# Optimization experiments

Measured on AMD Instinct MI355X. Metric: run time of the kernel, lower is better.

The kernel has to match this reference:

```python
import jax, jax.numpy as jnp
import numpy as np

B, N_NODES, VOCAB, H = 128, 1023, 2048, 256  # depth-9 perfect binary trees (heap layout)


def setup_inputs() -> dict:
    key = jax.random.key(0)
    k1, k2, k3, k4, k5 = jax.random.split(key, 5)
    tokens = jax.random.randint(k1, (B, N_NODES), 0, VOCAB)
    emb = jax.random.normal(k2, (VOCAB, H), dtype=jnp.float32) * 0.02
    Wx = jax.random.normal(k3, (H, 5 * H), dtype=jnp.float32) * 0.02
    Ul = jax.random.normal(k4, (H, 5 * H), dtype=jnp.float32) * 0.02
    Ur = jax.random.normal(k5, (H, 5 * H), dtype=jnp.float32) * 0.02
    b = jnp.zeros((5 * H,), dtype=jnp.float32)
    return {"tokens": tokens, "emb": emb, "Wx": Wx, "Ul": Ul, "Ur": Ur, "b": b}


def _tree_lstm(tokens, emb, Wx, Ul, Ur, b):
    # tokens: [B, 2^(D+1)-1] in level-order heap layout; children of heap index i
    # are 2i+1, 2i+2 -> within level d+1 they sit at offsets 2k, 2k+1.
    n_nodes = tokens.shape[1]
    depth = int(np.log2(n_nodes + 1)) - 1
    hdim = emb.shape[1]
    x_all = emb[tokens]  # [B, N, H] embedding lookup (memory-bound gather)
    h = c = None
    for d in range(depth, -1, -1):  # bottom-up over levels (fixed structural loop)
        start, n = 2 ** d - 1, 2 ** d
        x = x_all[:, start:start + n]  # [B, n, H]
        gates = jnp.einsum('bnh,hg->bng', x, Wx) + b
        if h is not None:
            hl, hr = h[:, 0::2], h[:, 1::2]
            cl, cr = c[:, 0::2], c[:, 1::2]
            gates = gates + jnp.einsum('bnh,hg->bng', hl, Ul) + jnp.einsum('bnh,hg->bng', hr, Ur)
        i, fl, fr, o, u = jnp.split(gates, 5, axis=-1)
        i, fl, fr, o = map(jax.nn.sigmoid, (i, fl, fr, o))
        u = jnp.tanh(u)
        c_new = i * u
        if c is not None:
            c_new = c_new + fl * cl + fr * cr
        c = c_new
        h = o * jnp.tanh(c)
    return h[:, 0], c[:, 0]  # root states, each [B, H]


def reference(tokens, emb, Wx, Ul, Ur, b):
    h_root, _ = _tree_lstm(tokens, emb, Wx, Ul, Ur, b)
    return h_root  # [B, H]
```

## Files before the change

### kernel.cpp

```cpp
#include <hip/hip_runtime.h>
#include <hip/hip_bf16.h>
#include <math.h>

#define B_SZ   128
#define HDIM   256
#define NG     1280
#define NNODES 1023
#define VOCAB  2048

typedef unsigned int uint32;
typedef short  short8v  __attribute__((ext_vector_type(8)));
typedef float  float4v  __attribute__((ext_vector_type(4)));

__device__ __forceinline__ float sigm(float x) {
    return 1.0f / (1.0f + __expf(-x));
}
__device__ __forceinline__ float tanh_fast(float x) {
    return 2.0f / (1.0f + __expf(-2.0f * x)) - 1.0f;
}
__device__ __forceinline__ float bf2f(unsigned short u) {
    return __uint_as_float(((uint32)u) << 16);
}
__device__ __forceinline__ unsigned short f2bf(float f) {
    uint32 x = __float_as_uint(f);
    uint32 r = (x + 0x7FFFu + ((x >> 16) & 1u)) >> 16;
    return (unsigned short)r;
}

__device__ __forceinline__ void dma16(const unsigned short* gptr, unsigned short* lptr) {
    __builtin_amdgcn_global_load_lds(
        (const __attribute__((address_space(1))) void*)gptr,
        (__attribute__((address_space(3))) void*)lptr, 16, 0, 0);
}

__global__ __launch_bounds__(256) void embb_kernel(
    const float* __restrict__ emb, unsigned short* __restrict__ embb)
{
    const int t = blockIdx.x * 256 + threadIdx.x;
    const float4 v0 = *(const float4*)(emb + (size_t)t * 8);
    const float4 v1 = *(const float4*)(emb + (size_t)t * 8 + 4);
    short8v o;
    o[0] = (short)f2bf(v0.x); o[1] = (short)f2bf(v0.y);
    o[2] = (short)f2bf(v0.z); o[3] = (short)f2bf(v0.w);
    o[4] = (short)f2bf(v1.x); o[5] = (short)f2bf(v1.y);
    o[6] = (short)f2bf(v1.z); o[7] = (short)f2bf(v1.w);
    *(short8v*)(embb + (size_t)t * 8) = o;
}

__global__ __launch_bounds__(256) void prep_wtf(
    const float* __restrict__ Ul, const float* __restrict__ Ur,
    const float* __restrict__ Wx, unsigned short* __restrict__ WTf)
{
    const int t = blockIdx.x * 256 + threadIdx.x;
    const int l = t & 63;
    const int q = l >> 4, c = l & 15;
    const int ks = (t >> 6) % 24;
    const int ng = t / (24 * 64);
    const int col = ng * 16 + c;
    const int k = ks * 32 + q * 8;
    const float* src = (k < 256) ? (Ul + (size_t)k * NG + col)
                     : (k < 512) ? (Ur + (size_t)(k - 256) * NG + col)
                                 : (Wx + (size_t)(k - 512) * NG + col);
    short8v v;
    #pragma unroll
    for (int j = 0; j < 8; ++j) v[j] = (short)f2bf(src[(size_t)j * NG]);
    *(short8v*)(WTf + (size_t)t * 8) = v;
}

__global__ __launch_bounds__(256, 2) void ewb_mfma(
    const unsigned short* __restrict__ WTf, const unsigned short* __restrict__ embb,
    const float* __restrict__ bias, unsigned short* __restrict__ EWb)
{
    __shared__ __align__(16) unsigned short Ab[2][4096];
    __shared__ __align__(16) unsigned short wbE[20480];

    const int tid  = threadIdx.x;
    const int lane = tid & 63;
    const int w    = tid >> 6;
    const int quad = lane >> 4, col15 = lane & 15;
    const int jt = blockIdx.x;
    const int rowBase = blockIdx.y * 64;
    const int jbase   = jt * 64;

    const unsigned short* agp[2];
    unsigned short* ldst[2];
    #pragma unroll
    for (int t = 0; t < 2; ++t) {
        const int ch = 2 * w + t, sub = ch >> 2, rt = ch & 3;
        const int srow = rowBase + rt * 16 + col15;
        agp[t]  = embb + (size_t)srow * HDIM + sub * 32 + quad * 8;
        ldst[t] = &Ab[0][0] + ch * 512;
    }

    const short8v* WTfv = (const short8v*)WTf;
    uint32 boff[5];
    #pragma unroll
    for (int g = 0; g < 5; ++g)
        boff[g] = ((g * 16 + jt * 4 + w) * 24 + 16) * 64 + lane;

    float4v acc[4][5];
    #pragma unroll
    for (int rt = 0; rt < 4; ++rt)
        #pragma unroll
        for (int g = 0; g < 5; ++g)
            #pragma unroll
            for (int e = 0; e < 4; ++e) acc[rt][g][e] = 0.0f;

    dma16(agp[0], ldst[0]); dma16(agp[1], ldst[1]);
    __syncthreads();

    #pragma unroll
    for (int s = 0; s < 4; ++s) {
        if (s < 3) {
            dma16(agp[0] + (s + 1) * 64, ldst[0] + ((s + 1) & 1) * 4096);
            dma16(agp[1] + (s + 1) * 64, ldst[1] + ((s + 1) & 1) * 4096);
        }
        #pragma unroll
        for (int sub = 0; sub < 2; ++sub) {
            short8v bf[5];
            #pragma unroll
            for (int g = 0; g < 5; ++g) bf[g] = WTfv[boff[g] + (s * 2 + sub) * 64];
            #pragma unroll
            for (int rt = 0; rt < 4; ++rt) {
                const short8v af = *(const short8v*)&Ab[s & 1][(sub * 4 + rt) * 512 + lane * 8];
                #pragma unroll
                for (int g = 0; g < 5; ++g)
                    acc[rt][g] = __builtin_amdgcn_mfma_f32_16x16x32_bf16(
                        af, bf[g], acc[rt][g], 0, 0, 0);
            }
        }
        __syncthreads();
    }

    const int jl = w * 16 + col15;
    const int j  = jbase + jl;
    float bz[5];
    #pragma unroll
    for (int g = 0; g < 5; ++g) bz[g] = bias[g * 256 + j];
    const int jchunk = jl >> 3, jpos = jl & 7;

    #pragma unroll
    for (int rt = 0; rt < 4; ++rt) {
        #pragma unroll
        for (int reg = 0; reg < 4; ++reg) {
            const int rr = rt * 16 + quad * 4 + reg;
            const int roff = ((jchunk + 2 * quad) & 7) * 8 + jpos;
            #pragma unroll
            for (int g = 0; g < 5; ++g)
                wbE[(g * 64 + rr) * 64 + roff] = f2bf(acc[rt][g][reg] + bz[g]);
        }
    }
    __syncthreads();

    #pragma unroll
    for (int k2 = 0; k2 < 10; ++k2) {
        const int c = tid + k2 * 256;
        const int g = c >> 9, rr = (c >> 3) & 63, u = c & 7;
        const int ru = (u + 2 * ((rr >> 2) & 3)) & 7;
        const short8v v = *(const short8v*)&wbE[(g * 64 + rr) * 64 + ru * 8];
        *(short8v*)(EWb + (size_t)(rowBase + rr) * NG + g * 256 + jbase + u * 8) = v;
    }
}

__global__ __launch_bounds__(256) void leaftab_kernel(
    const unsigned short* __restrict__ EWb,
    unsigned short* __restrict__ Hleaf, unsigned short* __restrict__ Cleaf)
{
    const int t = blockIdx.x * 256 + threadIdx.x;
    const int tok = t >> 8, j = t & 255;
    const float gi = bf2f(EWb[(size_t)tok * NG + j]);
    const float go = bf2f(EWb[(size_t)tok * NG + 768 + j]);
    const float gu = bf2f(EWb[(size_t)tok * NG + 1024 + j]);
    const float c = sigm(gi) * tanh_fast(gu);
    const float h = sigm(go) * tanh_fast(c);
    Hleaf[t] = f2bf(h);
    Cleaf[t] = f2bf(c);
}

template <bool LEAF>
__global__ __launch_bounds__(256, 2) void level_kernel(
    const unsigned short* __restrict__ WTf, const int* __restrict__ tokens,
    const unsigned short* __restrict__ embb,
    const unsigned short* __restrict__ Hleaf, const unsigned short* __restrict__ Cleaf,
    const unsigned short* __restrict__ hsrc, const unsigned short* __restrict__ csrc,
    const float* __restrict__ bias,
    unsigned short* __restrict__ hdst, unsigned short* __restrict__ cdst,
    float* __restrict__ out, const int d)
{
    const int n = 1 << d;

    __shared__ __align__(16) unsigned short Ab[2][8192];

    const int tid  = threadIdx.x;
    const int lane = tid & 63;
    const int w    = tid >> 6;
    const int quad = lane >> 4, col15 = lane & 15;
    const int jt = blockIdx.x;
    const int rowBase = blockIdx.y * 64;
    const int jbase   = jt * 64;

    const uint32 inrow = (uint32)(w * 64 + quad * 16);
    uint32 oL[4], oR[4], oN[4];
    #pragma unroll
    for (int t = 0; t < 4; ++t) {
        const int srow = rowBase + t * 16 + col15;
        const int b = srow >> d, i = srow & (n - 1);
        oN[t] = (uint32)tokens[b * NNODES + (n - 1) + i] * 512u + inrow;
        if (LEAF) {
            oL[t] = (uint32)tokens[b * NNODES + 511 + 2 * i] * 512u + inrow;
            oR[t] = (uint32)tokens[b * NNODES + 512 + 2 * i] * 512u + inrow;
        } else {
            oL[t] = (uint32)(2 * srow) * 512u + inrow;
            oR[t] = oL[t] + 512u;
        }
    }
    const char* hb = LEAF ? (const char*)Hleaf : (const char*)hsrc;
    const char* xb = (const char*)embb;

    const short8v* WTfv = (const short8v*)WTf;
    uint32 boff[5];
    #pragma unroll
    for (int g = 0; g < 5; ++g)
        boff[g] = ((g * 16 + jt * 4 + w) * 24) * 64 + lane;

    const int jl = w * 16 + col15;
    const int j  = jbase + jl;
    float bz[5];
    #pragma unroll
    for (int g = 0; g < 5; ++g) bz[g] = bias[g * 256 + j];

    float4v acc[4][5];
    #pragma unroll
    for (int rt = 0; rt < 4; ++rt)
        #pragma unroll
        for (int g = 0; g < 5; ++g)
            #pragma unroll
            for (int e = 0; e < 4; ++e) acc[rt][g][e] = 0.0f;

    {
        unsigned short* dst = &Ab[0][0] + w * 2048;
        #pragma unroll
        for (int t = 0; t < 4; ++t)
            dma16((const unsigned short*)(hb + oL[t]), dst + t * 512);
    }
    __syncthreads();

    #pragma unroll
    for (int s = 0; s < 6; ++s) {
        if (s < 5) {
            const int sn = s + 1;
            unsigned short* dst = &Ab[sn & 1][0] + w * 2048;
            #pragma unroll
            for (int t = 0; t < 4; ++t) {
                const char* p = (sn < 2) ? (hb + oL[t] + sn * 256)
                              : (sn < 4) ? (hb + oR[t] + (sn - 2) * 256)
                                         : (xb + oN[t] + (sn - 4) * 256);
                dma16((const unsigned short*)p, dst + t * 512);
            }
        }

        #pragma unroll
        for (int sub = 0; sub < 4; ++sub) {
            short8v bf[5];
            #pragma unroll
            for (int g = 0; g < 5; ++g) bf[g] = WTfv[boff[g] + (s * 4 + sub) * 64];
            #pragma unroll
            for (int rt = 0; rt < 4; ++rt) {
                const short8v af = *(const short8v*)&Ab[s & 1][(sub * 4 + rt) * 512 + lane * 8];
                #pragma unroll
                for (int g = 0; g < 5; ++g)
                    acc[rt][g] = __builtin_amdgcn_mfma_f32_16x16x32_bf16(
                        af, bf[g], acc[rt][g], 0, 0, 0);
            }
        }
        __syncthreads();
    }

    float hv[4][4], cv[4][4];
    #pragma unroll
    for (int rt = 0; rt < 4; ++rt) {
        #pragma unroll
        for (int reg = 0; reg < 4; ++reg) {
            const int rr = rt * 16 + quad * 4 + reg;
            const int grow = rowBase + rr;
            float cl, cr;
            if (LEAF) {
                const int b = grow >> 8, i = grow & 255;
                const int tokL = tokens[b * NNODES + 511 + 2 * i];
                const int tokR = tokens[b * NNODES + 512 + 2 * i];
                cl = bf2f(Cleaf[(size_t)tokL * HDIM + j]);
                cr = bf2f(Cleaf[(size_t)tokR * HDIM + j]);
            } else {
                cl = bf2f(csrc[(size_t)(2 * grow) * HDIM + j]);
                cr = bf2f(csrc[(size_t)(2 * grow + 1) * HDIM + j]);
            }
            const float gi  = acc[rt][0][reg] + bz[0];
            const float gfl = acc[rt][1][reg] + bz[1];
            const float gfr = acc[rt][2][reg] + bz[2];
            const float go  = acc[rt][3][reg] + bz[3];
            const float gu  = acc[rt][4][reg] + bz[4];
            const float ii = sigm(gi), fl = sigm(gfl), fr = sigm(gfr), oo = sigm(go);
            const float uu = tanh_fast(gu);
            const float c = ii * uu + fl * cl + fr * cr;
            const float h = oo * tanh_fast(c);
            cv[rt][reg] = c; hv[rt][reg] = h;
            if (!LEAF && d == 0) out[(size_t)grow * HDIM + j] = h;
        }
    }
    if (!LEAF && d == 0) return;

    unsigned short* wb = &Ab[0][0];
    const int jchunk = jl >> 3, jpos = jl & 7;
    #pragma unroll
    for (int rt = 0; rt < 4; ++rt) {
        #pragma unroll
        for (int reg = 0; reg < 4; ++reg) {
            const int rr = rt * 16 + quad * 4 + reg;
            const int roff = ((jchunk + 2 * quad) & 7) * 8 + jpos;
            wb[rr * 64 + roff]        = f2bf(hv[rt][reg]);
            wb[4096 + rr * 64 + roff] = f2bf(cv[rt][reg]);
        }
    }
    __syncthreads();
    #pragma unroll
    for (int k2 = 0; k2 < 4; ++k2) {
        const int c = tid + k2 * 256;
        const int arr = c >> 9, rr = (c >> 3) & 63, u = c & 7;
        const int ru = (u + 2 * ((rr >> 2) & 3)) & 7;
        const short8v v = *(const short8v*)(wb + (arr * 4096 + rr * 64 + ru * 8));
        unsigned short* dstp = (arr ? cdst : hdst) +
            (size_t)(rowBase + rr) * HDIM + jbase + u * 8;
        *(short8v*)dstp = v;
    }
}

extern "C" void kernel_launch(void* const* d_in, const int* in_sizes, int n_in,
                              void* d_out, int out_size, void* d_ws, size_t ws_size,
                              hipStream_t stream)
{
    const int*   tokens = (const int*)d_in[0];
    const float* emb    = (const float*)d_in[1];
    const float* Wx     = (const float*)d_in[2];
    const float* Ul     = (const float*)d_in[3];
    const float* Ur     = (const float*)d_in[4];
    const float* bias   = (const float*)d_in[5];
    float* out = (float*)d_out;

    const size_t EW_ELEMS  = (size_t)VOCAB * NG;
    const size_t EMB_ELEMS = (size_t)VOCAB * HDIM;
    const size_t WTF_ELEMS = (size_t)80 * 24 * 64 * 8;
    const size_t LT_ELEMS  = (size_t)VOCAB * HDIM;
    const size_t SLOT_A    = (size_t)16384 * HDIM;
    const size_t SLOT_B    = (size_t)32768 * HDIM;
    const size_t REQUIRED  = (EW_ELEMS + EMB_ELEMS + WTF_ELEMS + 2 * LT_ELEMS
                              + 2 * (SLOT_A + SLOT_B)) * 2;
    if (ws_size < REQUIRED || d_ws == nullptr) return;

    char* ws = (char*)d_ws;
    unsigned short* EWb   = (unsigned short*)ws;
    unsigned short* embb  = EWb + EW_ELEMS;
    unsigned short* WTf   = embb + EMB_ELEMS;
    unsigned short* Hleaf = WTf + WTF_ELEMS;
    unsigned short* Cleaf = Hleaf + LT_ELEMS;
    unsigned short* hA    = Cleaf + LT_ELEMS;
    unsigned short* cA    = hA + SLOT_A;
    unsigned short* hB    = cA + SLOT_A;
    unsigned short* cB    = hB + SLOT_B;

    embb_kernel<<<dim3(256), 256, 0, stream>>>(emb, embb);
    prep_wtf<<<dim3(480), 256, 0, stream>>>(Ul, Ur, Wx, WTf);
    ewb_mfma<<<dim3(4, 32), 256, 0, stream>>>(WTf, embb, bias, EWb);
    leaftab_kernel<<<dim3(2048), 256, 0, stream>>>(EWb, Hleaf, Cleaf);

    for (int d = 8; d >= 0; --d) {
        const int NRB = 2 << d;
        const bool evenD = ((d & 1) == 0);
        const unsigned short* hs = evenD ? hA : hB;
        const unsigned short* cs = evenD ? cA : cB;
        unsigned short* hd = evenD ? hB : hA;
        unsigned short* cd = evenD ? cB : cA;
        if (d == 8) {
            level_kernel<true><<<dim3(4, NRB), 256, 0, stream>>>(
                WTf, tokens, embb, Hleaf, Cleaf, hs, cs, bias, hd, cd, out, d);
        } else {
            level_kernel<false><<<dim3(4, NRB), 256, 0, stream>>>(
                WTf, tokens, embb, Hleaf, Cleaf, hs, cs, bias, hd, cd, out, d);
        }
    }
}
```

Measured before the change: 356.6 us.

## Fuse small upper tree levels into persistent kernel with grid barrier; gather precomputed x-gates

Levels 5..0 now run inside one persistent kernel of 256 blocks, separated by a software grid barrier. This replaces six small kernel launches whose cost is mostly launch overhead. Levels 8..6 no longer run the x-projection GEMM step and instead gather the precomputed per-token EWb gate rows in the epilogue, which cuts the K loop from 6 stages to 4. The grid barrier depends on all 256 blocks being co-resident, and the bf16-rounded EWb table adds a small precision difference.

New measurement: 1.292 ms. +262.3%, slower.

```diff
diff --git a/kernel.cpp b/kernel.cpp
--- a/kernel.cpp
+++ b/kernel.cpp
@@ -33,10 +33,30 @@
         (__attribute__((address_space(3))) void*)lptr, 16, 0, 0);
 }
 
+__device__ __forceinline__ void grid_barrier(unsigned* cnt, unsigned* gen, unsigned nb) {
+    __threadfence();
+    __syncthreads();
+    if (threadIdx.x == 0) {
+        unsigned g = __hip_atomic_load(gen, __ATOMIC_RELAXED, __HIP_MEMORY_SCOPE_AGENT);
+        unsigned a = __hip_atomic_fetch_add(cnt, 1u, __ATOMIC_ACQ_REL, __HIP_MEMORY_SCOPE_AGENT);
+        if (a == nb - 1u) {
+            __hip_atomic_store(cnt, 0u, __ATOMIC_RELAXED, __HIP_MEMORY_SCOPE_AGENT);
+            __hip_atomic_fetch_add(gen, 1u, __ATOMIC_RELEASE, __HIP_MEMORY_SCOPE_AGENT);
+        } else {
+            while (__hip_atomic_load(gen, __ATOMIC_ACQUIRE, __HIP_MEMORY_SCOPE_AGENT) == g)
+                __builtin_amdgcn_s_sleep(2);
+        }
+    }
+    __syncthreads();
+    __threadfence();
+}
+
 __global__ __launch_bounds__(256) void embb_kernel(
-    const float* __restrict__ emb, unsigned short* __restrict__ embb)
+    const float* __restrict__ emb, unsigned short* __restrict__ embb,
+    unsigned* __restrict__ bar)
 {
     const int t = blockIdx.x * 256 + threadIdx.x;
+    if (t == 0) { bar[0] = 0u; bar[1] = 0u; }
     const float4 v0 = *(const float4*)(emb + (size_t)t * 8);
     const float4 v1 = *(const float4*)(emb + (size_t)t * 8 + 4);
     short8v o;
@@ -178,14 +198,13 @@
 }
 
 template <bool LEAF>
-__global__ __launch_bounds__(256, 2) void level_kernel(
+__global__ __launch_bounds__(256, 2) void level_gather(
     const unsigned short* __restrict__ WTf, const int* __restrict__ tokens,
-    const unsigned short* __restrict__ embb,
+    const unsigned short* __restrict__ EWb,
     const unsigned short* __restrict__ Hleaf, const unsigned short* __restrict__ Cleaf,
     const unsigned short* __restrict__ hsrc, const unsigned short* __restrict__ csrc,
-    const float* __restrict__ bias,
     unsigned short* __restrict__ hdst, unsigned short* __restrict__ cdst,
-    float* __restrict__ out, const int d)
+    const int d)
 {
     const int n = 1 << d;
 
@@ -200,13 +219,12 @@
     const int jbase   = jt * 64;
 
     const uint32 inrow = (uint32)(w * 64 + quad * 16);
-    uint32 oL[4], oR[4], oN[4];
+    uint32 oL[4], oR[4];
     #pragma unroll
     for (int t = 0; t < 4; ++t) {
         const int srow = rowBase + t * 16 + col15;
-        const int b = srow >> d, i = srow & (n - 1);
-        oN[t] = (uint32)tokens[b * NNODES + (n - 1) + i] * 512u + inrow;
         if (LEAF) {
+            const int b = srow >> 8, i = srow & 255;
             oL[t] = (uint32)tokens[b * NNODES + 511 + 2 * i] * 512u + inrow;
             oR[t] = (uint32)tokens[b * NNODES + 512 + 2 * i] * 512u + inrow;
         } else {
@@ -215,7 +233,6 @@
         }
     }
     const char* hb = LEAF ? (const char*)Hleaf : (const char*)hsrc;
-    const char* xb = (const char*)embb;
 
     const short8v* WTfv = (const short8v*)WTf;
     uint32 boff[5];
@@ -223,12 +240,6 @@
     for (int g = 0; g < 5; ++g)
         boff[g] = ((g * 16 + jt * 4 + w) * 24) * 64 + lane;
 
-    const int jl = w * 16 + col15;
-    const int j  = jbase + jl;
-    float bz[5];
-    #pragma unroll
-    for (int g = 0; g < 5; ++g) bz[g] = bias[g * 256 + j];
-
     float4v acc[4][5];
     #pragma unroll
     for (int rt = 0; rt < 4; ++rt)
@@ -246,19 +257,17 @@
     __syncthreads();
 
     #pragma unroll
-    for (int s = 0; s < 6; ++s) {
-        if (s < 5) {
+    for (int s = 0; s < 4; ++s) {
+        if (s < 3) {
             const int sn = s + 1;
             unsigned short* dst = &Ab[sn & 1][0] + w * 2048;
             #pragma unroll
             for (int t = 0; t < 4; ++t) {
                 const char* p = (sn < 2) ? (hb + oL[t] + sn * 256)
-                              : (sn < 4) ? (hb + oR[t] + (sn - 2) * 256)
-                                         : (xb + oN[t] + (sn - 4) * 256);
+                                         : (hb + oR[t] + (sn - 2) * 256);
                 dma16((const unsigned short*)p, dst + t * 512);
             }
         }
-
         #pragma unroll
         for (int sub = 0; sub < 4; ++sub) {
             short8v bf[5];
@@ -276,6 +285,8 @@
         __syncthreads();
     }
 
+    const int jl = w * 16 + col15;
+    const int j  = jbase + jl;
     float hv[4][4], cv[4][4];
     #pragma unroll
     for (int rt = 0; rt < 4; ++rt) {
@@ -283,6 +294,8 @@
         for (int reg = 0; reg < 4; ++reg) {
             const int rr = rt * 16 + quad * 4 + reg;
             const int grow = rowBase + rr;
+            const int tok = tokens[(grow >> d) * NNODES + (n - 1) + (grow & (n - 1))];
+            const unsigned short* ewp = EWb + (size_t)tok * NG + j;
             float cl, cr;
             if (LEAF) {
                 const int b = grow >> 8, i = grow & 255;
@@ -294,23 +307,22 @@
                 cl = bf2f(csrc[(size_t)(2 * grow) * HDIM + j]);
                 cr = bf2f(csrc[(size_t)(2 * grow + 1) * HDIM + j]);
             }
-            const float gi  = acc[rt][0][reg] + bz[0];
-            const float gfl = acc[rt][1][reg] + bz[1];
-            const float gfr = acc[rt][2][reg] + bz[2];
-            const float go  = acc[rt][3][reg] + bz[3];
-            const float gu  = acc[rt][4][reg] + bz[4];
+            const float gi  = acc[rt][0][reg] + bf2f(ewp[0]);
+            const float gfl = acc[rt][1][reg] + bf2f(ewp[256]);
+            const float gfr = acc[rt][2][reg] + bf2f(ewp[512]);
+            const float go  = acc[rt][3][reg] + bf2f(ewp[768]);
+            const float gu  = acc[rt][4][reg] + bf2f(ewp[1024]);
             const float ii = sigm(gi), fl = sigm(gfl), fr = sigm(gfr), oo = sigm(go);
             const float uu = tanh_fast(gu);
             const float c = ii * uu + fl * cl + fr * cr;
             const float h = oo * tanh_fast(c);
             cv[rt][reg] = c; hv[rt][reg] = h;
-            if (!LEAF && d == 0) out[(size_t)grow * HDIM + j] = h;
-        }
-    }
-    if (!LEAF && d == 0) return;
+        }
+    }
 
     unsigned short* wb = &Ab[0][0];
     const int jchunk = jl >> 3, jpos = jl & 7;
+    __syncthreads();
     #pragma unroll
     for (int rt = 0; rt < 4; ++rt) {
         #pragma unroll
@@ -334,6 +346,162 @@
     }
 }
 
+__global__ __launch_bounds__(256, 2) void level_fused(
+    const unsigned short* __restrict__ WTf, const int* __restrict__ tokens,
+    const unsigned short* __restrict__ embb,
+    unsigned short* __restrict__ hA, unsigned short* __restrict__ cA,
+    unsigned short* __restrict__ hB, unsigned short* __restrict__ cB,
+    const float* __restrict__ bias, float* __restrict__ out,
+    unsigned* __restrict__ bar)
+{
+    __shared__ __align__(16) unsigned short Ab[2][8192];
+
+    const int tid  = threadIdx.x;
+    const int lane = tid & 63;
+    const int w    = tid >> 6;
+    const int quad = lane >> 4, col15 = lane & 15;
+    const int bid  = blockIdx.x;
+    const int jt   = bid & 3;
+    const int jbase = jt * 64;
+    const int jl = w * 16 + col15;
+    const int j  = jbase + jl;
+    const uint32 inrow = (uint32)(w * 64 + quad * 16);
+
+    float bz[5];
+    #pragma unroll
+    for (int g = 0; g < 5; ++g) bz[g] = bias[g * 256 + j];
+
+    const short8v* WTfv = (const short8v*)WTf;
+    uint32 boff[5];
+    #pragma unroll
+    for (int g = 0; g < 5; ++g)
+        boff[g] = ((g * 16 + jt * 4 + w) * 24) * 64 + lane;
+
+    const char* xb = (const char*)embb;
+
+    #pragma unroll 1
+    for (int d = 5; d >= 0; --d) {
+        const unsigned short *hsv, *csv;
+        unsigned short *hdv, *cdv;
+        if (d & 1) { hsv = hB; csv = cB; hdv = hA; cdv = cA; }
+        else       { hsv = hA; csv = cA; hdv = hB; cdv = cB; }
+        const int n = 1 << d;
+        const int nact = 8 << d;
+
+        if (bid < nact) {
+            const int rowBase = (bid >> 2) * 64;
+
+            uint32 oL[4], oR[4], oN[4];
+            #pragma unroll
+            for (int t = 0; t < 4; ++t) {
+                const int srow = rowBase + t * 16 + col15;
+                const int b = srow >> d, i = srow & (n - 1);
+                oN[t] = (uint32)tokens[b * NNODES + (n - 1) + i] * 512u + inrow;
+                oL[t] = (uint32)(2 * srow) * 512u + inrow;
+                oR[t] = oL[t] + 512u;
+            }
+            const char* hb = (const char*)hsv;
+
+            float4v acc[4][5];
+            #pragma unroll
+            for (int rt = 0; rt < 4; ++rt)
+                #pragma unroll
+                for (int g = 0; g < 5; ++g)
+                    #pragma unroll
+                    for (int e = 0; e < 4; ++e) acc[rt][g][e] = 0.0f;
+
+            {
+                unsigned short* dst = &Ab[0][0] + w * 2048;
+                #pragma unroll
+                for (int t = 0; t < 4; ++t)
+                    dma16((const unsigned short*)(hb + oL[t]), dst + t * 512);
+            }
+            __syncthreads();
+
+            #pragma unroll
+            for (int s = 0; s < 6; ++s) {
+                if (s < 5) {
+                    const int sn = s + 1;
+                    unsigned short* dst = &Ab[sn & 1][0] + w * 2048;
+                    #pragma unroll
+                    for (int t = 0; t < 4; ++t) {
+                        const char* p = (sn < 2) ? (hb + oL[t] + sn * 256)
+                                      : (sn < 4) ? (hb + oR[t] + (sn - 2) * 256)
+                                                 : (xb + oN[t] + (sn - 4) * 256);
+                        dma16((const unsigned short*)p, dst + t * 512);
+                    }
+                }
+                #pragma unroll
+                for (int sub = 0; sub < 4; ++sub) {
+                    short8v bf[5];
+                    #pragma unroll
+                    for (int g = 0; g < 5; ++g) bf[g] = WTfv[boff[g] + (s * 4 + sub) * 64];
+                    #pragma unroll
+                    for (int rt = 0; rt < 4; ++rt) {
+                        const short8v af = *(const short8v*)&Ab[s & 1][(sub * 4 + rt) * 512 + lane * 8];
+                        #pragma unroll
+                        for (int g = 0; g < 5; ++g)
+                            acc[rt][g] = __builtin_amdgcn_mfma_f32_16x16x32_bf16(
+                                af, bf[g], acc[rt][g], 0, 0, 0);
+                    }
+                }
+                __syncthreads();
+            }
+
+            float hv[4][4], cv[4][4];
+            #pragma unroll
+            for (int rt = 0; rt < 4; ++rt) {
+                #pragma unroll
+                for (int reg = 0; reg < 4; ++reg) {
+                    const int rr = rt * 16 + quad * 4 + reg;
+                    const int grow = rowBase + rr;
+                    const float cl = bf2f(csv[(size_t)(2 * grow) * HDIM + j]);
+                    const float cr = bf2f(csv[(size_t)(2 * grow + 1) * HDIM + j]);
+                    const float gi  = acc[rt][0][reg] + bz[0];
+                    const float gfl = acc[rt][1][reg] + bz[1];
+                    const float gfr = acc[rt][2][reg] + bz[2];
+                    const float go  = acc[rt][3][reg] + bz[3];
+                    const float gu  = acc[rt][4][reg] + bz[4];
+                    const float ii = sigm(gi), fl = sigm(gfl), fr = sigm(gfr), oo = sigm(go);
+                    const float uu = tanh_fast(gu);
+                    const float c = ii * uu + fl * cl + fr * cr;
+                    const float h = oo * tanh_fast(c);
+                    cv[rt][reg] = c; hv[rt][reg] = h;
+                    if (d == 0) out[(size_t)grow * HDIM + j] = h;
+                }
+            }
+
+            if (d > 0) {
+                unsigned short* wb = &Ab[0][0];
+                const int jchunk = jl >> 3, jpos = jl & 7;
+                #pragma unroll
+                for (int rt = 0; rt < 4; ++rt) {
+                    #pragma unroll
+                    for (int reg = 0; reg < 4; ++reg) {
+                        const int rr = rt * 16 + quad * 4 + reg;
+                        const int roff = ((jchunk + 2 * quad) & 7) * 8 + jpos;
+                        wb[rr * 64 + roff]        = f2bf(hv[rt][reg]);
+                        wb[4096 + rr * 64 + roff] = f2bf(cv[rt][reg]);
+                    }
+                }
+                __syncthreads();
+                #pragma unroll
+                for (int k2 = 0; k2 < 4; ++k2) {
+                    const int c = tid + k2 * 256;
+                    const int arr = c >> 9, rr = (c >> 3) & 63, u = c & 7;
+                    const int ru = (u + 2 * ((rr >> 2) & 3)) & 7;
+                    const short8v v = *(const short8v*)(wb + (arr * 4096 + rr * 64 + ru * 8));
+                    unsigned short* dstp = (arr ? cdv : hdv) +
+                        (size_t)(rowBase + rr) * HDIM + jbase + u * 8;
+                    *(short8v*)dstp = v;
+                }
+            }
+        }
+
+        if (d > 0) grid_barrier(bar, bar + 1, gridDim.x);
+    }
+}
+
 extern "C" void kernel_launch(void* const* d_in, const int* in_sizes, int n_in,
                               void* d_out, int out_size, void* d_ws, size_t ws_size,
                               hipStream_t stream)
@@ -353,7 +521,7 @@
     const size_t SLOT_A    = (size_t)16384 * HDIM;
     const size_t SLOT_B    = (size_t)32768 * HDIM;
     const size_t REQUIRED  = (EW_ELEMS + EMB_ELEMS + WTF_ELEMS + 2 * LT_ELEMS
-                              + 2 * (SLOT_A + SLOT_B)) * 2;
+                              + 2 * (SLOT_A + SLOT_B)) * 2 + 64;
     if (ws_size < REQUIRED || d_ws == nullptr) return;
 
     char* ws = (char*)d_ws;
@@ -366,25 +534,20 @@
     unsigned short* cA    = hA + SLOT_A;
     unsigned short* hB    = cA + SLOT_A;
     unsigned short* cB    = hB + SLOT_B;
-
-    embb_kernel<<<dim3(256), 256, 0, stream>>>(emb, embb);
+    unsigned* bar         = (unsigned*)(cB + SLOT_B);
+
+    embb_kernel<<<dim3(256), 256, 0, stream>>>(emb, embb, bar);
     prep_wtf<<<dim3(480), 256, 0, stream>>>(Ul, Ur, Wx, WTf);
     ewb_mfma<<<dim3(4, 32), 256, 0, stream>>>(WTf, embb, bias, EWb);
     leaftab_kernel<<<dim3(2048), 256, 0, stream>>>(EWb, Hleaf, Cleaf);
 
-    for (int d = 8; d >= 0; --d) {
-        const int NRB = 2 << d;
-        const bool evenD = ((d & 1) == 0);
-        const unsigned short* hs = evenD ? hA : hB;
-        const unsigned short* cs = evenD ? cA : cB;
-        unsigned short* hd = evenD ? hB : hA;
-        unsigned short* cd = evenD ? cB : cA;
-        if (d == 8) {
-            level_kernel<true><<<dim3(4, NRB), 256, 0, stream>>>(
-                WTf, tokens, embb, Hleaf, Cleaf, hs, cs, bias, hd, cd, out, d);
-        } else {
-            level_kernel<false><<<dim3(4, NRB), 256, 0, stream>>>(
-                WTf, tokens, embb, Hleaf, Cleaf, hs, cs, bias, hd, cd, out, d);
-        }
-    }
-}
+    level_gather<true><<<dim3(4, 512), 256, 0, stream>>>(
+        WTf, tokens, EWb, Hleaf, Cleaf, nullptr, nullptr, hB, cB, 8);
+    level_gather<false><<<dim3(4, 256), 256, 0, stream>>>(
+        WTf, tokens, EWb, Hleaf, Cleaf, hB, cB, hA, cA, 7);
+    level_gather<false><<<dim3(4, 128), 256, 0, stream>>>(
+        WTf, tokens, EWb, Hleaf, Cleaf, hA, cA, hB, cB, 6);
+
+    level_fused<<<dim3(256), 256, 0, stream>>>(
+        WTf, tokens, embb, hA, cA, hB, cB, bias, out, bar);
+}
```

## Precompute per-token leaf recurrent projections and replace leaf-parent GEMM with gather

Applied to the files above, without the earlier changes.

Because leaf hidden states depend only on the token, the recurrent projections Hleaf·Ul and Hleaf·Ur are precomputed once per vocabulary entry with the existing GEMM kernel, generalized by a K-slice offset and optional bias. The level just above the leaves is then computed by an elementwise kernel that gathers and sums three precomputed gate rows per node. This replaces the largest level's full GEMM with table gathers. The cost is two extra vocab-sized tables, additional workspace, and more scattered memory reads.

Measured after the change: 331.6 us. 7.0% less time.

```diff
diff --git a/kernel.cpp b/kernel.cpp
--- a/kernel.cpp
+++ b/kernel.cpp
@@ -67,9 +67,10 @@
     *(short8v*)(WTf + (size_t)t * 8) = v;
 }
 
-__global__ __launch_bounds__(256, 2) void ewb_mfma(
-    const unsigned short* __restrict__ WTf, const unsigned short* __restrict__ embb,
-    const float* __restrict__ bias, unsigned short* __restrict__ EWb)
+__global__ __launch_bounds__(256, 2) void gemm_tab(
+    const unsigned short* __restrict__ WTf, const unsigned short* __restrict__ A,
+    const float* __restrict__ bias, unsigned short* __restrict__ O,
+    const int ks_base)
 {
     __shared__ __align__(16) unsigned short Ab[2][4096];
     __shared__ __align__(16) unsigned short wbE[20480];
@@ -88,7 +89,7 @@
     for (int t = 0; t < 2; ++t) {
         const int ch = 2 * w + t, sub = ch >> 2, rt = ch & 3;
         const int srow = rowBase + rt * 16 + col15;
-        agp[t]  = embb + (size_t)srow * HDIM + sub * 32 + quad * 8;
+        agp[t]  = A + (size_t)srow * HDIM + sub * 32 + quad * 8;
         ldst[t] = &Ab[0][0] + ch * 512;
     }
 
@@ -96,7 +97,7 @@
     uint32 boff[5];
     #pragma unroll
     for (int g = 0; g < 5; ++g)
-        boff[g] = ((g * 16 + jt * 4 + w) * 24 + 16) * 64 + lane;
+        boff[g] = (uint32)(((g * 16 + jt * 4 + w) * 24 + ks_base) * 64 + lane);
 
     float4v acc[4][5];
     #pragma unroll
@@ -136,7 +137,7 @@
     const int j  = jbase + jl;
     float bz[5];
     #pragma unroll
-    for (int g = 0; g < 5; ++g) bz[g] = bias[g * 256 + j];
+    for (int g = 0; g < 5; ++g) bz[g] = bias ? bias[g * 256 + j] : 0.0f;
     const int jchunk = jl >> 3, jpos = jl & 7;
 
     #pragma unroll
@@ -158,7 +159,7 @@
         const int g = c >> 9, rr = (c >> 3) & 63, u = c & 7;
         const int ru = (u + 2 * ((rr >> 2) & 3)) & 7;
         const short8v v = *(const short8v*)&wbE[(g * 64 + rr) * 64 + ru * 8];
-        *(short8v*)(EWb + (size_t)(rowBase + rr) * NG + g * 256 + jbase + u * 8) = v;
+        *(short8v*)(O + (size_t)(rowBase + rr) * NG + g * 256 + jbase + u * 8) = v;
     }
 }
 
@@ -177,11 +178,57 @@
     Cleaf[t] = f2bf(c);
 }
 
-template <bool LEAF>
-__global__ __launch_bounds__(256, 2) void level_kernel(
+__global__ __launch_bounds__(256) void leafcell_kernel(
+    const int* __restrict__ tokens,
+    const unsigned short* __restrict__ HUl, const unsigned short* __restrict__ HUr,
+    const unsigned short* __restrict__ EWb, const unsigned short* __restrict__ Cleaf,
+    unsigned short* __restrict__ hdst, unsigned short* __restrict__ cdst)
+{
+    const int t = blockIdx.x * 256 + threadIdx.x;
+    const int row = t >> 5;
+    const int j   = (t & 31) * 8;
+    const int b = row >> 8, i = row & 255;
+    const int tokN = tokens[b * NNODES + 255 + i];
+    const int tokL = tokens[b * NNODES + 511 + 2 * i];
+    const int tokR = tokens[b * NNODES + 512 + 2 * i];
+
+    const unsigned short* pl = HUl + (size_t)tokL * NG + j;
+    const unsigned short* pr = HUr + (size_t)tokR * NG + j;
+    const unsigned short* pn = EWb + (size_t)tokN * NG + j;
+
+    float g5[5][8];
+    #pragma unroll
+    for (int g = 0; g < 5; ++g) {
+        const short8v vl = *(const short8v*)(pl + g * 256);
+        const short8v vr = *(const short8v*)(pr + g * 256);
+        const short8v vn = *(const short8v*)(pn + g * 256);
+        #pragma unroll
+        for (int e = 0; e < 8; ++e)
+            g5[g][e] = bf2f((unsigned short)vl[e]) + bf2f((unsigned short)vr[e])
+                     + bf2f((unsigned short)vn[e]);
+    }
+    const short8v cl8 = *(const short8v*)(Cleaf + (size_t)tokL * HDIM + j);
+    const short8v cr8 = *(const short8v*)(Cleaf + (size_t)tokR * HDIM + j);
+
+    short8v ho, co;
+    #pragma unroll
+    for (int e = 0; e < 8; ++e) {
+        const float ii = sigm(g5[0][e]), fl = sigm(g5[1][e]);
+        const float fr = sigm(g5[2][e]), oo = sigm(g5[3][e]);
+        const float uu = tanh_fast(g5[4][e]);
+        const float c = ii * uu + fl * bf2f((unsigned short)cl8[e])
+                                + fr * bf2f((unsigned short)cr8[e]);
+        const float h = oo * tanh_fast(c);
+        co[e] = (short)f2bf(c);
+        ho[e] = (short)f2bf(h);
+    }
+    *(short8v*)(hdst + (size_t)row * HDIM + j) = ho;
+    *(short8v*)(cdst + (size_t)row * HDIM + j) = co;
+}
+
+__global__ __launch_bounds__(256, 2) void level_fold(
     const unsigned short* __restrict__ WTf, const int* __restrict__ tokens,
     const unsigned short* __restrict__ embb,
-    const unsigned short* __restrict__ Hleaf, const unsigned short* __restrict__ Cleaf,
     const unsigned short* __restrict__ hsrc, const unsigned short* __restrict__ csrc,
     const float* __restrict__ bias,
     unsigned short* __restrict__ hdst, unsigned short* __restrict__ cdst,
@@ -206,15 +253,10 @@
         const int srow = rowBase + t * 16 + col15;
         const int b = srow >> d, i = srow & (n - 1);
         oN[t] = (uint32)tokens[b * NNODES + (n - 1) + i] * 512u + inrow;
-        if (LEAF) {
-            oL[t] = (uint32)tokens[b * NNODES + 511 + 2 * i] * 512u + inrow;
-            oR[t] = (uint32)tokens[b * NNODES + 512 + 2 * i] * 512u + inrow;
-        } else {
-            oL[t] = (uint32)(2 * srow) * 512u + inrow;
-            oR[t] = oL[t] + 512u;
-        }
-    }
-    const char* hb = LEAF ? (const char*)Hleaf : (const char*)hsrc;
+        oL[t] = (uint32)(2 * srow) * 512u + inrow;
+        oR[t] = oL[t] + 512u;
+    }
+    const char* hb = (const char*)hsrc;
     const char* xb = (const char*)embb;
 
     const short8v* WTfv = (const short8v*)WTf;
@@ -258,7 +300,6 @@
                 dma16((const unsigned short*)p, dst + t * 512);
             }
         }
-
         #pragma unroll
         for (int sub = 0; sub < 4; ++sub) {
             short8v bf[5];
@@ -283,17 +324,8 @@
         for (int reg = 0; reg < 4; ++reg) {
             const int rr = rt * 16 + quad * 4 + reg;
             const int grow = rowBase + rr;
-            float cl, cr;
-            if (LEAF) {
-                const int b = grow >> 8, i = grow & 255;
-                const int tokL = tokens[b * NNODES + 511 + 2 * i];
-                const int tokR = tokens[b * NNODES + 512 + 2 * i];
-                cl = bf2f(Cleaf[(size_t)tokL * HDIM + j]);
-                cr = bf2f(Cleaf[(size_t)tokR * HDIM + j]);
-            } else {
-                cl = bf2f(csrc[(size_t)(2 * grow) * HDIM + j]);
-                cr = bf2f(csrc[(size_t)(2 * grow + 1) * HDIM + j]);
-            }
+            const float cl = bf2f(csrc[(size_t)(2 * grow) * HDIM + j]);
+            const float cr = bf2f(csrc[(size_t)(2 * grow + 1) * HDIM + j]);
             const float gi  = acc[rt][0][reg] + bz[0];
             const float gfl = acc[rt][1][reg] + bz[1];
             const float gfr = acc[rt][2][reg] + bz[2];
@@ -304,10 +336,10 @@
             const float c = ii * uu + fl * cl + fr * cr;
             const float h = oo * tanh_fast(c);
             cv[rt][reg] = c; hv[rt][reg] = h;
-            if (!LEAF && d == 0) out[(size_t)grow * HDIM + j] = h;
-        }
-    }
-    if (!LEAF && d == 0) return;
+            if (d == 0) out[(size_t)grow * HDIM + j] = h;
+        }
+    }
+    if (d == 0) return;
 
     unsigned short* wb = &Ab[0][0];
     const int jchunk = jl >> 3, jpos = jl & 7;
@@ -352,13 +384,15 @@
     const size_t LT_ELEMS  = (size_t)VOCAB * HDIM;
     const size_t SLOT_A    = (size_t)16384 * HDIM;
     const size_t SLOT_B    = (size_t)32768 * HDIM;
-    const size_t REQUIRED  = (EW_ELEMS + EMB_ELEMS + WTF_ELEMS + 2 * LT_ELEMS
+    const size_t REQUIRED  = (3 * EW_ELEMS + EMB_ELEMS + WTF_ELEMS + 2 * LT_ELEMS
                               + 2 * (SLOT_A + SLOT_B)) * 2;
     if (ws_size < REQUIRED || d_ws == nullptr) return;
 
     char* ws = (char*)d_ws;
     unsigned short* EWb   = (unsigned short*)ws;
-    unsigned short* embb  = EWb + EW_ELEMS;
+    unsigned short* HUl   = EWb + EW_ELEMS;
+    unsigned short* HUr   = HUl + EW_ELEMS;
+    unsigned short* embb  = HUr + EW_ELEMS;
     unsigned short* WTf   = embb + EMB_ELEMS;
     unsigned short* Hleaf = WTf + WTF_ELEMS;
     unsigned short* Cleaf = Hleaf + LT_ELEMS;
@@ -369,22 +403,22 @@
 
     embb_kernel<<<dim3(256), 256, 0, stream>>>(emb, embb);
     prep_wtf<<<dim3(480), 256, 0, stream>>>(Ul, Ur, Wx, WTf);
-    ewb_mfma<<<dim3(4, 32), 256, 0, stream>>>(WTf, embb, bias, EWb);
+    gemm_tab<<<dim3(4, 32), 256, 0, stream>>>(WTf, embb, bias, EWb, 16);
     leaftab_kernel<<<dim3(2048), 256, 0, stream>>>(EWb, Hleaf, Cleaf);
-
-    for (int d = 8; d >= 0; --d) {
+    gemm_tab<<<dim3(4, 32), 256, 0, stream>>>(WTf, Hleaf, nullptr, HUl, 0);
+    gemm_tab<<<dim3(4, 32), 256, 0, stream>>>(WTf, Hleaf, nullptr, HUr, 8);
+
+    leafcell_kernel<<<dim3(4096), 256, 0, stream>>>(
+        tokens, HUl, HUr, EWb, Cleaf, hB, cB);
+
+    for (int d = 7; d >= 0; --d) {
         const int NRB = 2 << d;
         const bool evenD = ((d & 1) == 0);
         const unsigned short* hs = evenD ? hA : hB;
         const unsigned short* cs = evenD ? cA : cB;
         unsigned short* hd = evenD ? hB : hA;
         unsigned short* cd = evenD ? cB : cA;
-        if (d == 8) {
-            level_kernel<true><<<dim3(4, NRB), 256, 0, stream>>>(
-                WTf, tokens, embb, Hleaf, Cleaf, hs, cs, bias, hd, cd, out, d);
-        } else {
-            level_kernel<false><<<dim3(4, NRB), 256, 0, stream>>>(
-                WTf, tokens, embb, Hleaf, Cleaf, hs, cs, bias, hd, cd, out, d);
-        }
-    }
-}
+        level_fold<<<dim3(4, NRB), 256, 0, stream>>>(
+            WTf, tokens, embb, hs, cs, bias, hd, cd, out, d);
+    }
+}
```
